# Performance work log

Measured on AMD Instinct MI355X. Metric: run time of the kernel, lower is better.

## Reference

```python
import jax, jax.numpy as jnp
import numpy as np

H = 1024      # hidden_size
V = 50257     # output_size (vocab)


def setup_inputs() -> dict:
    key = jax.random.key(0)
    ks = jax.random.split(key, 9)
    s = 1.0 / np.sqrt(H)
    return {
        "input_ids": jax.random.randint(ks[0], (1,), 0, V, dtype=jnp.int64)
        if jax.config.jax_enable_x64 else jax.random.randint(ks[0], (1,), 0, V, dtype=jnp.int32),
        "hidden": jax.random.normal(ks[1], (1, 1, H), dtype=jnp.float32),
        "emb": jax.random.normal(ks[2], (V, H), dtype=jnp.float32),
        "W_ih": jax.random.uniform(ks[3], (3 * H, H), jnp.float32, -s, s),
        "W_hh": jax.random.uniform(ks[4], (3 * H, H), jnp.float32, -s, s),
        "b_ih": jax.random.uniform(ks[5], (3 * H,), jnp.float32, -s, s),
        "b_hh": jax.random.uniform(ks[6], (3 * H,), jnp.float32, -s, s),
        "W_out": jax.random.uniform(ks[7], (V, H), jnp.float32, -s, s),
        "b_out": jax.random.uniform(ks[8], (V,), jnp.float32, -s, s),
    }


def gru_cell(x, h, W_ih, W_hh, b_ih, b_hh):
    # x, h: [B, H]; PyTorch GRU gate ordering: r, z, n
    gi = x @ W_ih.T + b_ih           # [B, 3H]
    gh = h @ W_hh.T + b_hh           # [B, 3H]
    i_r, i_z, i_n = jnp.split(gi, 3, axis=-1)
    h_r, h_z, h_n = jnp.split(gh, 3, axis=-1)
    r = jax.nn.sigmoid(i_r + h_r)
    z = jax.nn.sigmoid(i_z + h_z)
    n = jnp.tanh(i_n + r * h_n)
    return (1.0 - z) * n + z * h


def reference(input_ids, hidden, emb, W_ih, W_hh, b_ih, b_hh, W_out, b_out):
    # embedding lookup -> [1, 1, H] (seq=1, batch=1)
    x = emb[input_ids].reshape(1, 1, H)
    x = jax.nn.relu(x)
    # single-step, single-layer GRU (n_layers = 1 in the original intent)
    h_new = gru_cell(x[0], hidden[0], W_ih, W_hh, b_ih, b_hh)   # [1, H]
    hidden_out = h_new[None]                                    # [1, 1, H]
    logits = h_new @ W_out.T + b_out                            # [1, V]
    logp = jax.nn.log_softmax(logits, axis=-1)
    return logp, hidden_out
```

## Files before the change

### kernel.cpp

```cpp
#include <hip/hip_runtime.h>
#include <math.h>

#define H 1024
#define V 50257
#define NTILES 6283
#define NBLK 512
#define GBLK 512
#define NB_FINAL 64

__device__ __forceinline__ float wave_reduce_sum(float v) {
#pragma unroll
    for (int off = 32; off >= 1; off >>= 1)
        v += __shfl_xor(v, off, 64);
    return v;
}

__device__ __forceinline__ void sm_merge(float& m, float& s, float mi, float si) {
    if (mi > m) {
        s = s * expf(m - mi) + si;
        m = mi;
    } else if (si > 0.f) {
        s += si * expf(mi - m);
    }
}

__global__ __launch_bounds__(256) void gru_fused_kernel(
    const int* __restrict__ ids, const float* __restrict__ emb,
    const float* __restrict__ hidden,
    const float* __restrict__ W_ih, const float* __restrict__ W_hh,
    const float* __restrict__ b_ih, const float* __restrict__ b_hh,
    float* __restrict__ hnew, float* __restrict__ out_hidden)
{
    const int b = blockIdx.x;
    const int t = threadIdx.x;
    const int wave = t >> 6;
    const int lane = t & 63;

    float pbi[3], pbh[3], ph = 0.f;
    if (t < 2) {
        const int j = 2 * b + t;
        pbi[0] = b_ih[j]; pbi[1] = b_ih[H + j]; pbi[2] = b_ih[2*H + j];
        pbh[0] = b_hh[j]; pbh[1] = b_hh[H + j]; pbh[2] = b_hh[2*H + j];
        ph = hidden[j];
    }

    const int id = ids[0];
    float4 x4 = ((const float4*)(emb + (size_t)id * H))[t];
    const float4 h4 = ((const float4*)hidden)[t];

    float4 w[12];
#pragma unroll
    for (int jj = 0; jj < 2; ++jj) {
        const int j = 2 * b + jj;
#pragma unroll
        for (int g = 0; g < 3; ++g) {
            w[jj*6 + 2*g]     = ((const float4*)(W_ih + ((size_t)g * H + j) * H))[t];
            w[jj*6 + 2*g + 1] = ((const float4*)(W_hh + ((size_t)g * H + j) * H))[t];
        }
    }

    x4.x = fmaxf(x4.x, 0.f); x4.y = fmaxf(x4.y, 0.f);
    x4.z = fmaxf(x4.z, 0.f); x4.w = fmaxf(x4.w, 0.f);

    float acc[12];
#pragma unroll
    for (int k = 0; k < 12; ++k) {
        const float4 v = w[k];
        const float4 u = (k & 1) ? h4 : x4;
        acc[k] = v.x * u.x + v.y * u.y + v.z * u.z + v.w * u.w;
    }
#pragma unroll
    for (int k = 0; k < 12; ++k) acc[k] = wave_reduce_sum(acc[k]);

    __shared__ float red[4][12];
    if (lane == 0) {
#pragma unroll
        for (int k = 0; k < 12; ++k) red[wave][k] = acc[k];
    }
    __syncthreads();
    if (t < 2) {
        float tt[6];
#pragma unroll
        for (int k = 0; k < 6; ++k) {
            const int c = t * 6 + k;
            tt[k] = red[0][c] + red[1][c] + red[2][c] + red[3][c];
        }
        const int j = 2 * b + t;
        const float ir  = tt[0] + pbi[0],  hr_ = tt[1] + pbh[0];
        const float iz  = tt[2] + pbi[1],  hz  = tt[3] + pbh[1];
        const float in_ = tt[4] + pbi[2],  hn  = tt[5] + pbh[2];
        const float r = 1.f / (1.f + expf(-(ir + hr_)));
        const float z = 1.f / (1.f + expf(-(iz + hz)));
        const float n = tanhf(in_ + r * hn);
        const float o = (1.f - z) * n + z * ph;
        hnew[j] = o;
        out_hidden[j] = o;
    }
}


#define LOADT(W, BO, tile) do {                                               \
    const int _b = (tile) * 8 + wave * 2;                                     \
    _Pragma("unroll")                                                         \
    for (int _r = 0; _r < 2; ++_r) {                                          \
        const int _row = (_b + _r < V) ? (_b + _r) : (V - 1);                 \
        const float4* _w = (const float4*)(W_out + (size_t)_row * H);         \
        _Pragma("unroll")                                                     \
        for (int _it = 0; _it < 4; ++_it) W[_r][_it] = _w[_it * 64 + lane];   \
        BO[_r] = b_out[_row];                                                 \
    }                                                                         \
} while (0)

#define COMPUTET(W, BO, tile) do {                                            \
    const int _b = (tile) * 8 + wave * 2;                                     \
    float _acc[2];                                                            \
    _Pragma("unroll")                                                         \
    for (int _r = 0; _r < 2; ++_r) {                                          \
        _acc[_r] = W[_r][0].x * hreg[0].x + W[_r][0].y * hreg[0].y            \
                 + W[_r][0].z * hreg[0].z + W[_r][0].w * hreg[0].w            \
                 + W[_r][1].x * hreg[1].x + W[_r][1].y * hreg[1].y            \
                 + W[_r][1].z * hreg[1].z + W[_r][1].w * hreg[1].w            \
                 + W[_r][2].x * hreg[2].x + W[_r][2].y * hreg[2].y            \
                 + W[_r][2].z * hreg[2].z + W[_r][2].w * hreg[2].w            \
                 + W[_r][3].x * hreg[3].x + W[_r][3].y * hreg[3].y            \
                 + W[_r][3].z * hreg[3].z + W[_r][3].w * hreg[3].w;           \
    }                                                                         \
    _Pragma("unroll")                                                         \
    for (int _r = 0; _r < 2; ++_r) _acc[_r] = wave_reduce_sum(_acc[_r]);      \
    if (lane == 0) {                                                          \
        _Pragma("unroll")                                                     \
        for (int _r = 0; _r < 2; ++_r) {                                      \
            const int _row = _b + _r;                                         \
            if (_row < V) {                                                   \
                const float _lg = _acc[_r] + BO[_r];                          \
                logits[_row] = _lg;                                           \
                sm_merge(m, s, _lg, 1.f);                                     \
            }                                                                 \
        }                                                                     \
    }                                                                         \
} while (0)

__global__ __launch_bounds__(256, 4) void logits_persistent_kernel(
    const float* __restrict__ hnew, const float* __restrict__ W_out,
    const float* __restrict__ b_out, float* __restrict__ logits,
    float* __restrict__ pmax, float* __restrict__ psum)
{
    __shared__ float wm[4], wsv[4];
    const int wave = threadIdx.x >> 6;
    const int lane = threadIdx.x & 63;
    const int bid  = blockIdx.x;

    float4 hreg[4];
#pragma unroll
    for (int it = 0; it < 4; ++it)
        hreg[it] = ((const float4*)hnew)[it * 64 + lane];

    float m = -INFINITY, s = 0.f;

    float4 wA[2][4], wB[2][4];
    float boA[2], boB[2];
    int t = bid;
    LOADT(wA, boA, t);
    for (;;) {
        const int tn = t + NBLK;
        const bool vn = tn < NTILES;
        if (vn) LOADT(wB, boB, tn);
        COMPUTET(wA, boA, t);
        if (!vn) break;
        const int tn2 = tn + NBLK;
        const bool vn2 = tn2 < NTILES;
        if (vn2) LOADT(wA, boA, tn2);
        COMPUTET(wB, boB, tn);
        if (!vn2) break;
        t = tn2;
    }

    if (lane == 0) { wm[wave] = m; wsv[wave] = s; }
    __syncthreads();
    if (threadIdx.x == 0) {
        float M = wm[0], S = wsv[0];
#pragma unroll
        for (int w2 = 1; w2 < 4; ++w2) sm_merge(M, S, wm[w2], wsv[w2]);
        pmax[bid] = M;
        psum[bid] = S;
    }
}

__global__ __launch_bounds__(256) void finalize_kernel(
    const float* __restrict__ pmax, const float* __restrict__ psum,
    float* __restrict__ out)
{
    __shared__ float wm[4], wsv[4];
    __shared__ float total_s;
    const int tid = threadIdx.x;

    float m = -INFINITY, s = 0.f;
    for (int i = tid; i < NBLK; i += 256)
        sm_merge(m, s, pmax[i], psum[i]);
#pragma unroll
    for (int off = 32; off >= 1; off >>= 1) {
        const float mo = __shfl_xor(m, off, 64);
        const float so = __shfl_xor(s, off, 64);
        sm_merge(m, s, mo, so);
    }
    if ((tid & 63) == 0) { wm[tid >> 6] = m; wsv[tid >> 6] = s; }
    __syncthreads();
    if (tid == 0) {
        float M = wm[0], S = wsv[0];
#pragma unroll
        for (int w2 = 1; w2 < 4; ++w2) sm_merge(M, S, wm[w2], wsv[w2]);
        total_s = M + logf(S);
    }
    __syncthreads();
    const float t = total_s;

    float4* out4 = (float4*)out;
    const int n4 = V / 4;
    for (int i = blockIdx.x * 256 + tid; i < n4; i += NB_FINAL * 256) {
        float4 v = out4[i];
        v.x -= t; v.y -= t; v.z -= t; v.w -= t;
        out4[i] = v;
    }
    if (blockIdx.x == 0 && tid == 0) out[V - 1] -= t;
}

extern "C" void kernel_launch(void* const* d_in, const int* in_sizes, int n_in,
                              void* d_out, int out_size, void* d_ws, size_t ws_size,
                              hipStream_t stream) {
    const int*   ids    = (const int*)  d_in[0];
    const float* hidden = (const float*)d_in[1];
    const float* emb    = (const float*)d_in[2];
    const float* W_ih   = (const float*)d_in[3];
    const float* W_hh   = (const float*)d_in[4];
    const float* b_ih   = (const float*)d_in[5];
    const float* b_hh   = (const float*)d_in[6];
    const float* W_out  = (const float*)d_in[7];
    const float* b_out  = (const float*)d_in[8];

    float* out = (float*)d_out;

    float* ws   = (float*)d_ws;
    float* hnew = ws;
    float* pmax = ws + H;
    float* psum = pmax + NBLK;

    gru_fused_kernel<<<GBLK, 256, 0, stream>>>(ids, emb, hidden, W_ih, W_hh,
                                               b_ih, b_hh, hnew, out + V);
    logits_persistent_kernel<<<NBLK, 256, 0, stream>>>(hnew, W_out, b_out, out,
                                                       pmax, psum);
    finalize_kernel<<<NB_FINAL, 256, 0, stream>>>(pmax, psum, out);
}
```

Measured before the change: 48.17 us.

## Fuse GRU cell into persistent logits kernel with a grid-wide atomic barrier

```diff
diff --git a/kernel.cpp b/kernel.cpp
--- a/kernel.cpp
+++ b/kernel.cpp
@@ -5,8 +5,14 @@
 #define V 50257
 #define NTILES 6283
 #define NBLK 512
-#define GBLK 512
 #define NB_FINAL 64
+
+typedef float f32x4 __attribute__((ext_vector_type(4)));
+
+__device__ __forceinline__ float4 ntload4(const float* p) {
+    f32x4 v = __builtin_nontemporal_load((const f32x4*)p);
+    return make_float4(v.x, v.y, v.z, v.w);
+}
 
 __device__ __forceinline__ float wave_reduce_sum(float v) {
 #pragma unroll
@@ -24,89 +30,15 @@
     }
 }
 
-__global__ __launch_bounds__(256) void gru_fused_kernel(
-    const int* __restrict__ ids, const float* __restrict__ emb,
-    const float* __restrict__ hidden,
-    const float* __restrict__ W_ih, const float* __restrict__ W_hh,
-    const float* __restrict__ b_ih, const float* __restrict__ b_hh,
-    float* __restrict__ hnew, float* __restrict__ out_hidden)
-{
-    const int b = blockIdx.x;
-    const int t = threadIdx.x;
-    const int wave = t >> 6;
-    const int lane = t & 63;
-
-    float pbi[3], pbh[3], ph = 0.f;
-    if (t < 2) {
-        const int j = 2 * b + t;
-        pbi[0] = b_ih[j]; pbi[1] = b_ih[H + j]; pbi[2] = b_ih[2*H + j];
-        pbh[0] = b_hh[j]; pbh[1] = b_hh[H + j]; pbh[2] = b_hh[2*H + j];
-        ph = hidden[j];
-    }
-
-    const int id = ids[0];
-    float4 x4 = ((const float4*)(emb + (size_t)id * H))[t];
-    const float4 h4 = ((const float4*)hidden)[t];
-
-    float4 w[12];
-#pragma unroll
-    for (int jj = 0; jj < 2; ++jj) {
-        const int j = 2 * b + jj;
-#pragma unroll
-        for (int g = 0; g < 3; ++g) {
-            w[jj*6 + 2*g]     = ((const float4*)(W_ih + ((size_t)g * H + j) * H))[t];
-            w[jj*6 + 2*g + 1] = ((const float4*)(W_hh + ((size_t)g * H + j) * H))[t];
-        }
-    }
-
-    x4.x = fmaxf(x4.x, 0.f); x4.y = fmaxf(x4.y, 0.f);
-    x4.z = fmaxf(x4.z, 0.f); x4.w = fmaxf(x4.w, 0.f);
-
-    float acc[12];
-#pragma unroll
-    for (int k = 0; k < 12; ++k) {
-        const float4 v = w[k];
-        const float4 u = (k & 1) ? h4 : x4;
-        acc[k] = v.x * u.x + v.y * u.y + v.z * u.z + v.w * u.w;
-    }
-#pragma unroll
-    for (int k = 0; k < 12; ++k) acc[k] = wave_reduce_sum(acc[k]);
-
-    __shared__ float red[4][12];
-    if (lane == 0) {
-#pragma unroll
-        for (int k = 0; k < 12; ++k) red[wave][k] = acc[k];
-    }
-    __syncthreads();
-    if (t < 2) {
-        float tt[6];
-#pragma unroll
-        for (int k = 0; k < 6; ++k) {
-            const int c = t * 6 + k;
-            tt[k] = red[0][c] + red[1][c] + red[2][c] + red[3][c];
-        }
-        const int j = 2 * b + t;
-        const float ir  = tt[0] + pbi[0],  hr_ = tt[1] + pbh[0];
-        const float iz  = tt[2] + pbi[1],  hz  = tt[3] + pbh[1];
-        const float in_ = tt[4] + pbi[2],  hn  = tt[5] + pbh[2];
-        const float r = 1.f / (1.f + expf(-(ir + hr_)));
-        const float z = 1.f / (1.f + expf(-(iz + hz)));
-        const float n = tanhf(in_ + r * hn);
-        const float o = (1.f - z) * n + z * ph;
-        hnew[j] = o;
-        out_hidden[j] = o;
-    }
-}
-
-
 #define LOADT(W, BO, tile) do {                                               \
     const int _b = (tile) * 8 + wave * 2;                                     \
     _Pragma("unroll")                                                         \
     for (int _r = 0; _r < 2; ++_r) {                                          \
         const int _row = (_b + _r < V) ? (_b + _r) : (V - 1);                 \
-        const float4* _w = (const float4*)(W_out + (size_t)_row * H);         \
+        const float* _w = W_out + (size_t)_row * H;                           \
         _Pragma("unroll")                                                     \
-        for (int _it = 0; _it < 4; ++_it) W[_r][_it] = _w[_it * 64 + lane];   \
+        for (int _it = 0; _it < 4; ++_it)                                     \
+            W[_r][_it] = ntload4(_w + (_it * 64 + lane) * 4);                 \
         BO[_r] = b_out[_row];                                                 \
     }                                                                         \
 } while (0)
@@ -140,15 +72,104 @@
     }                                                                         \
 } while (0)
 
-__global__ __launch_bounds__(256, 4) void logits_persistent_kernel(
-    const float* __restrict__ hnew, const float* __restrict__ W_out,
-    const float* __restrict__ b_out, float* __restrict__ logits,
-    float* __restrict__ pmax, float* __restrict__ psum)
+__global__ __launch_bounds__(256, 4) void decoder_main_kernel(
+    const int* __restrict__ ids, const float* __restrict__ emb,
+    const float* __restrict__ hidden,
+    const float* __restrict__ W_ih, const float* __restrict__ W_hh,
+    const float* __restrict__ b_ih, const float* __restrict__ b_hh,
+    const float* __restrict__ W_out, const float* __restrict__ b_out,
+    float* __restrict__ logits, float* __restrict__ out_hidden,
+    float* __restrict__ hnew,
+    float* __restrict__ pmax, float* __restrict__ psum,
+    unsigned int* __restrict__ cnt)
 {
+    const int t256 = threadIdx.x;
+    const int wave = t256 >> 6;
+    const int lane = t256 & 63;
+    const int bid  = blockIdx.x;
+
+    __shared__ float red[4][12];
     __shared__ float wm[4], wsv[4];
-    const int wave = threadIdx.x >> 6;
-    const int lane = threadIdx.x & 63;
-    const int bid  = blockIdx.x;
+
+    {
+        float pbi0 = 0.f, pbi1 = 0.f, pbi2 = 0.f;
+        float pbh0 = 0.f, pbh1 = 0.f, pbh2 = 0.f, ph = 0.f;
+        if (t256 < 2) {
+            const int j = 2 * bid + t256;
+            pbi0 = b_ih[j]; pbi1 = b_ih[H + j]; pbi2 = b_ih[2*H + j];
+            pbh0 = b_hh[j]; pbh1 = b_hh[H + j]; pbh2 = b_hh[2*H + j];
+            ph = hidden[j];
+        }
+
+        const int id = ids[0];
+        float4 x4 = ((const float4*)(emb + (size_t)id * H))[t256];
+        const float4 h4 = ((const float4*)hidden)[t256];
+
+        float4 w[12];
+#pragma unroll
+        for (int jj = 0; jj < 2; ++jj) {
+            const int j = 2 * bid + jj;
+#pragma unroll
+            for (int g = 0; g < 3; ++g) {
+                w[jj*6 + 2*g]     = ntload4(W_ih + ((size_t)g * H + j) * H + 4 * t256);
+                w[jj*6 + 2*g + 1] = ntload4(W_hh + ((size_t)g * H + j) * H + 4 * t256);
+            }
+        }
+
+        x4.x = fmaxf(x4.x, 0.f); x4.y = fmaxf(x4.y, 0.f);
+        x4.z = fmaxf(x4.z, 0.f); x4.w = fmaxf(x4.w, 0.f);
+
+        float acc[12];
+#pragma unroll
+        for (int k = 0; k < 12; ++k) {
+            const float4 v = w[k];
+            const float4 u = (k & 1) ? h4 : x4;
+            acc[k] = v.x * u.x + v.y * u.y + v.z * u.z + v.w * u.w;
+        }
+#pragma unroll
+        for (int k = 0; k < 12; ++k) acc[k] = wave_reduce_sum(acc[k]);
+
+        if (lane == 0) {
+#pragma unroll
+            for (int k = 0; k < 12; ++k) red[wave][k] = acc[k];
+        }
+        __syncthreads();
+        if (t256 < 2) {
+            float tt[6];
+#pragma unroll
+            for (int k = 0; k < 6; ++k) {
+                const int c = t256 * 6 + k;
+                tt[k] = red[0][c] + red[1][c] + red[2][c] + red[3][c];
+            }
+            const int j = 2 * bid + t256;
+            const float ir  = tt[0] + pbi0,  hr_ = tt[1] + pbh0;
+            const float iz  = tt[2] + pbi1,  hz  = tt[3] + pbh1;
+            const float in_ = tt[4] + pbi2,  hn  = tt[5] + pbh2;
+            const float r = 1.f / (1.f + expf(-(ir + hr_)));
+            const float z = 1.f / (1.f + expf(-(iz + hz)));
+            const float n = tanhf(in_ + r * hn);
+            const float o = (1.f - z) * n + z * ph;
+            hnew[j] = o;
+            out_hidden[j] = o;
+        }
+    }
+
+    __builtin_amdgcn_fence(__ATOMIC_RELEASE, "agent");
+    __syncthreads();
+    if (t256 == 0)
+        __hip_atomic_fetch_add(cnt, 1u, __ATOMIC_RELEASE, __HIP_MEMORY_SCOPE_AGENT);
+
+    float4 wA[2][4], wB[2][4];
+    float boA[2], boB[2];
+    int tt = bid;
+    LOADT(wA, boA, tt);
+
+    if (t256 == 0) {
+        while (__hip_atomic_load(cnt, __ATOMIC_ACQUIRE, __HIP_MEMORY_SCOPE_AGENT) < NBLK)
+            __builtin_amdgcn_s_sleep(16);
+    }
+    __syncthreads();
+    __builtin_amdgcn_fence(__ATOMIC_ACQUIRE, "agent");
 
     float4 hreg[4];
 #pragma unroll
@@ -157,27 +178,23 @@
 
     float m = -INFINITY, s = 0.f;
 
-    float4 wA[2][4], wB[2][4];
-    float boA[2], boB[2];
-    int t = bid;
-    LOADT(wA, boA, t);
     for (;;) {
-        const int tn = t + NBLK;
+        const int tn = tt + NBLK;
         const bool vn = tn < NTILES;
         if (vn) LOADT(wB, boB, tn);
-        COMPUTET(wA, boA, t);
+        COMPUTET(wA, boA, tt);
         if (!vn) break;
         const int tn2 = tn + NBLK;
         const bool vn2 = tn2 < NTILES;
         if (vn2) LOADT(wA, boA, tn2);
         COMPUTET(wB, boB, tn);
         if (!vn2) break;
-        t = tn2;
+        tt = tn2;
     }
 
     if (lane == 0) { wm[wave] = m; wsv[wave] = s; }
     __syncthreads();
-    if (threadIdx.x == 0) {
+    if (t256 == 0) {
         float M = wm[0], S = wsv[0];
 #pragma unroll
         for (int w2 = 1; w2 < 4; ++w2) sm_merge(M, S, wm[w2], wsv[w2]);
@@ -243,10 +260,12 @@
     float* hnew = ws;
     float* pmax = ws + H;
     float* psum = pmax + NBLK;
-
-    gru_fused_kernel<<<GBLK, 256, 0, stream>>>(ids, emb, hidden, W_ih, W_hh,
-                                               b_ih, b_hh, hnew, out + V);
-    logits_persistent_kernel<<<NBLK, 256, 0, stream>>>(hnew, W_out, b_out, out,
-                                                       pmax, psum);
+    unsigned int* cnt = (unsigned int*)(psum + NBLK);
+
+    (void)hipMemsetAsync((void*)cnt, 0, sizeof(unsigned int), stream);
+
+    decoder_main_kernel<<<NBLK, 256, 0, stream>>>(
+        ids, emb, hidden, W_ih, W_hh, b_ih, b_hh, W_out, b_out,
+        out, out + V, hnew, pmax, psum, cnt);
     finalize_kernel<<<NB_FINAL, 256, 0, stream>>>(pmax, psum, out);
 }
```

New measurement: 123.3 us. +156.0%, slower.
